# Kernel tuning notes

Hardware: AMD Instinct MI355X
Metric: run time of the kernel (lower is better)

## Reference

```python
import jax, jax.numpy as jnp
import numpy as np

N_NODES = 50000
N_EDGES = 800000
NODE_DIM = 128
EDGE_DIM = 32
HID = 64
NEG_SLOPE = 0.2  # PyG GATConv default


def _gat_layer(x, src, dst, edge_attr, W, We, a_src, a_dst, a_edge, b, n_nodes):
    """PyG GATConv with heads=1, add_self_loops=True, fill_value='mean'."""
    h = x @ W                      # [N, H] node transform (bias=False in PyG)
    he = edge_attr @ We            # [E, H] edge transform
    # self-loop edge attr = mean of incoming edge_attr per node; linearity lets
    # us take the segment-mean of the transformed he instead.
    deg = jax.ops.segment_sum(jnp.ones((src.shape[0],), h.dtype), dst, num_segments=n_nodes)
    he_loop = jax.ops.segment_sum(he, dst, num_segments=n_nodes) / jnp.maximum(deg, 1.0)[:, None]
    loop = jnp.arange(n_nodes)
    src_a = jnp.concatenate([src, loop])
    dst_a = jnp.concatenate([dst, loop])
    he_a = jnp.concatenate([he, he_loop], axis=0)
    s_src = h @ a_src              # [N]
    s_dst = h @ a_dst              # [N]
    logits = jax.nn.leaky_relu(s_src[src_a] + s_dst[dst_a] + he_a @ a_edge, NEG_SLOPE)
    # segment softmax over destination nodes (every node has a self loop)
    m = jax.ops.segment_max(logits, dst_a, num_segments=n_nodes)
    ex = jnp.exp(logits - m[dst_a])
    denom = jax.ops.segment_sum(ex, dst_a, num_segments=n_nodes)
    alpha = ex / denom[dst_a]
    out = jax.ops.segment_sum(alpha[:, None] * h[src_a], dst_a, num_segments=n_nodes)
    return out + b


def setup_inputs() -> dict:
    key = jax.random.key(0)
    ks = jax.random.split(key, 20)
    s = 0.05
    inp = {
        "x": jax.random.normal(ks[0], (N_NODES, NODE_DIM), jnp.float32),
        "edge_index": jax.random.randint(ks[1], (2, N_EDGES), 0, N_NODES, jnp.int64 if jax.config.jax_enable_x64 else jnp.int32).astype(jnp.int32),
        "edge_attr": jax.random.normal(ks[2], (N_EDGES, EDGE_DIM), jnp.float32),
        "W1": jax.random.normal(ks[3], (NODE_DIM, HID)) * s,
        "We1": jax.random.normal(ks[4], (EDGE_DIM, HID)) * s,
        "as1": jax.random.normal(ks[5], (HID,)) * s,
        "ad1": jax.random.normal(ks[6], (HID,)) * s,
        "ae1": jax.random.normal(ks[7], (HID,)) * s,
        "b1": jnp.zeros((HID,)),
        "W2": jax.random.normal(ks[8], (HID, HID)) * s,
        "We2": jax.random.normal(ks[9], (EDGE_DIM, HID)) * s,
        "as2": jax.random.normal(ks[10], (HID,)) * s,
        "ad2": jax.random.normal(ks[11], (HID,)) * s,
        "ae2": jax.random.normal(ks[12], (HID,)) * s,
        "b2": jnp.zeros((HID,)),
        "Wc1": jax.random.normal(ks[13], (2 * HID + EDGE_DIM, HID)) * s,
        "bc1": jnp.zeros((HID,)),
        "Wc2": jax.random.normal(ks[14], (HID, 1)) * s,
        "bc2": jnp.zeros((1,)),
    }
    return inp


def reference(x, edge_index, edge_attr, W1, We1, as1, ad1, ae1, b1,
              W2, We2, as2, ad2, ae2, b2, Wc1, bc1, Wc2, bc2):
    n_nodes = x.shape[0]
    row, col = edge_index[0], edge_index[1]
    x1 = jax.nn.relu(_gat_layer(x, row, col, edge_attr, W1, We1, as1, ad1, ae1, b1, n_nodes))
    x2 = jax.nn.relu(_gat_layer(x1, row, col, edge_attr, W2, We2, as2, ad2, ae2, b2, n_nodes))
    ef = jnp.concatenate([x2[row], x2[col], edge_attr], axis=-1)  # [E, 2H+De]
    h = jax.nn.relu(ef @ Wc1 + bc1)
    return (h @ Wc2 + bc2)[:, 0]
```

## Files before the change

### kernel.cpp

```cpp
#include <hip/hip_runtime.h>
#include <hip/hip_bf16.h>

#define NODE_DIM 128
#define EDGE_DIM 32
#define HID 64
#define NEG_SLOPE 0.2f

typedef __attribute__((ext_vector_type(8))) short bf16x8;
typedef __attribute__((ext_vector_type(4))) float f32x4;


template <int CTRL, int RM, int BM>
__device__ __forceinline__ float dpp_mov(float v) {
    return __int_as_float(__builtin_amdgcn_update_dpp(
        __float_as_int(v), __float_as_int(v), CTRL, RM, BM, false));
}

__device__ __forceinline__ float wave_sum63(float v) {
    v += dpp_mov<0x111, 0xf, 0xf>(v);
    v += dpp_mov<0x112, 0xf, 0xf>(v);
    v += dpp_mov<0x114, 0xf, 0xe>(v);
    v += dpp_mov<0x118, 0xf, 0xc>(v);
    v += dpp_mov<0x142, 0xa, 0xf>(v);
    v += dpp_mov<0x143, 0xc, 0xf>(v);
    return v;
}

__device__ __forceinline__ float row16_sum15(float v) {
    v += dpp_mov<0x111, 0xf, 0xf>(v);
    v += dpp_mov<0x112, 0xf, 0xf>(v);
    v += dpp_mov<0x114, 0xf, 0xe>(v);
    v += dpp_mov<0x118, 0xf, 0xc>(v);
    return v;
}

__device__ __forceinline__ float bcast63(float v) {
    return __int_as_float(__builtin_amdgcn_readlane(__float_as_int(v), 63));
}

__device__ __forceinline__ unsigned short f2bf(float f) {
    unsigned u = __float_as_uint(f);
    unsigned r = (u + 0x7fffu + ((u >> 16) & 1u)) >> 16;
    return (unsigned short)r;
}
__device__ __forceinline__ float bf2f(unsigned short h) {
    return __uint_as_float(((unsigned)h) << 16);
}


__global__ void k_count_rank_t12(const int* __restrict__ col, int* __restrict__ deg,
                                 int* __restrict__ rank, const float* __restrict__ ea,
                                 const float* __restrict__ wea1,
                                 const float* __restrict__ wea2,
                                 float2* __restrict__ t12, int E) {
    int e = blockIdx.x * 256 + threadIdx.x;
    if (e >= E) return;
    rank[e] = atomicAdd(&deg[col[e]], 1);
    const float4* e4 = (const float4*)(ea + (size_t)e * EDGE_DIM);
    const float4* w1 = (const float4*)wea1;
    const float4* w2 = (const float4*)wea2;
    float t1 = 0.f, t2 = 0.f;
#pragma unroll
    for (int k = 0; k < EDGE_DIM / 4; k++) {
        float4 v = e4[k], a = w1[k], b = w2[k];
        t1 += v.x * a.x + v.y * a.y + v.z * a.z + v.w * a.w;
        t2 += v.x * b.x + v.y * b.y + v.z * b.z + v.w * b.w;
    }
    t12[e] = make_float2(t1, t2);
}

#define SCAN_B 256
__global__ void k_scan1(const int* __restrict__ deg, int* __restrict__ tmp,
                        int* __restrict__ bsum, int N) {
    __shared__ int s[SCAN_B];
    int i = blockIdx.x * SCAN_B + threadIdx.x;
    int v = (i < N) ? deg[i] : 0;
    s[threadIdx.x] = v;
    __syncthreads();
    for (int o = 1; o < SCAN_B; o <<= 1) {
        int t = (threadIdx.x >= o) ? s[threadIdx.x - o] : 0;
        __syncthreads();
        s[threadIdx.x] += t;
        __syncthreads();
    }
    if (i < N) tmp[i] = s[threadIdx.x];
    if (threadIdx.x == SCAN_B - 1) bsum[blockIdx.x] = s[threadIdx.x];
}

__global__ void k_scan2(int* __restrict__ bsum, int nb) {
    __shared__ int s[SCAN_B];
    int v = (threadIdx.x < nb) ? bsum[threadIdx.x] : 0;
    s[threadIdx.x] = v;
    __syncthreads();
    for (int o = 1; o < SCAN_B; o <<= 1) {
        int t = (threadIdx.x >= o) ? s[threadIdx.x - o] : 0;
        __syncthreads();
        s[threadIdx.x] += t;
        __syncthreads();
    }
    if (threadIdx.x < nb) bsum[threadIdx.x] = s[threadIdx.x] - v;
}

__global__ void k_scan3(const int* __restrict__ tmp, const int* __restrict__ deg,
                        const int* __restrict__ bsum, int* __restrict__ off, int N) {
    int i = blockIdx.x * SCAN_B + threadIdx.x;
    if (i < N) off[i] = tmp[i] - deg[i] + bsum[blockIdx.x];
}

__global__ void k_wea2(const float* __restrict__ We1, const float* __restrict__ ae1,
                       const float* __restrict__ We2, const float* __restrict__ ae2,
                       float* __restrict__ wea1, float* __restrict__ wea2) {
    int t = threadIdx.x;
    const float* We = (t < 32) ? We1 : We2;
    const float* ae = (t < 32) ? ae1 : ae2;
    float* o = (t < 32) ? wea1 : wea2;
    int k = t & 31;
    float s = 0.f;
#pragma unroll
    for (int j = 0; j < HID; j++) s += We[k * HID + j] * ae[j];
    o[k] = s;
}

__global__ void k_fill_pack(const int* __restrict__ row, const int* __restrict__ col,
                            const int* __restrict__ off, const int* __restrict__ rank,
                            const float2* __restrict__ t12, const float* __restrict__ ss1,
                            float4* __restrict__ pk, int E) {
    int e = blockIdx.x * 256 + threadIdx.x;
    if (e >= E) return;
    int dn = col[e];
    int p = off[dn] + rank[e];
    float2 t = t12[e];
    int sr = row[e];
    pk[p] = make_float4(t.x, t.y, __int_as_float(sr), t.x + ss1[sr]);
}

template <int K, int NT, bool ATT, bool PQ>
__global__ __launch_bounds__(256) void k_gemm_mfma(
    const float* __restrict__ X, const float* __restrict__ W,
    const float* __restrict__ as_, const float* __restrict__ ad_,
    unsigned short* __restrict__ H, unsigned short* __restrict__ H2,
    float* __restrict__ ss, float* __restrict__ sd, int N) {
    constexpr int KC = K / 32;
    int wv = threadIdx.x >> 6, lane = threadIdx.x & 63;
    int g = lane >> 4, li = lane & 15;
    bf16x8 bhi[KC][NT], blo[KC][NT];
#pragma unroll
    for (int c = 0; c < KC; c++)
#pragma unroll
        for (int t = 0; t < NT; t++)
#pragma unroll
            for (int j = 0; j < 8; j++) {
                int k = 32 * c + 8 * g + j;
                size_t idx = (size_t)(k + ((PQ && t >= 4) ? HID : 0)) * HID + 16 * (t & 3) + li;
                float w = W[idx];
                unsigned short h = f2bf(w);
                bhi[c][t][j] = (short)h;
                blo[c][t][j] = (short)f2bf(w - bf2f(h));
            }
    float asl[NT], adl[NT];
    if (ATT) {
#pragma unroll
        for (int t = 0; t < NT; t++) {
            asl[t] = as_[16 * t + li];
            adl[t] = ad_[16 * t + li];
        }
    }
    int ntile = (N + 15) >> 4;
    for (int tb = blockIdx.x * 4 + wv; tb < ntile; tb += gridDim.x * 4) {
        int node = tb * 16 + li;
        if (node >= N) node = N - 1;
        const float* xrow = X + (size_t)node * K;
        bf16x8 ahi[KC], alo[KC];
#pragma unroll
        for (int c = 0; c < KC; c++) {
            float4 a0 = *(const float4*)(xrow + 32 * c + 8 * g);
            float4 a1 = *(const float4*)(xrow + 32 * c + 8 * g + 4);
            float xv[8] = {a0.x, a0.y, a0.z, a0.w, a1.x, a1.y, a1.z, a1.w};
#pragma unroll
            for (int j = 0; j < 8; j++) {
                unsigned short h = f2bf(xv[j]);
                ahi[c][j] = (short)h;
                alo[c][j] = (short)f2bf(xv[j] - bf2f(h));
            }
        }
        f32x4 acc[NT];
#pragma unroll
        for (int t = 0; t < NT; t++) acc[t] = (f32x4){0.f, 0.f, 0.f, 0.f};
#pragma unroll
        for (int c = 0; c < KC; c++) {
#pragma unroll
            for (int t = 0; t < NT; t++)
                acc[t] = __builtin_amdgcn_mfma_f32_16x16x32_bf16(ahi[c], bhi[c][t], acc[t], 0, 0, 0);
#pragma unroll
            for (int t = 0; t < NT; t++)
                acc[t] = __builtin_amdgcn_mfma_f32_16x16x32_bf16(ahi[c], blo[c][t], acc[t], 0, 0, 0);
#pragma unroll
            for (int t = 0; t < NT; t++)
                acc[t] = __builtin_amdgcn_mfma_f32_16x16x32_bf16(alo[c], bhi[c][t], acc[t], 0, 0, 0);
        }
        int nbase = tb * 16 + 4 * g;
#pragma unroll
        for (int t = 0; t < NT; t++) {
            unsigned short* dst = (PQ && t >= 4) ? H2 : H;
            int cofs = 16 * (t & 3) + li;
#pragma unroll
            for (int r = 0; r < 4; r++) {
                int n = nbase + r;
                if (n < N) dst[(size_t)n * HID + cofs] = f2bf(acc[t][r]);
            }
        }
        if (ATT) {
#pragma unroll
            for (int r = 0; r < 4; r++) {
                float s1 = 0.f, s2 = 0.f;
#pragma unroll
                for (int t = 0; t < NT; t++) {
                    s1 += acc[t][r] * asl[t];
                    s2 += acc[t][r] * adl[t];
                }
                s1 = row16_sum15(s1);
                s2 = row16_sum15(s2);
                int n = nbase + r;
                if (li == 15 && n < N) {
                    ss[n] = s1;
                    sd[n] = s2;
                }
            }
        }
    }
}

template <bool FOLD>
__global__ __launch_bounds__(256) void k_aggregate(
    const unsigned short* __restrict__ H, const float* __restrict__ ss,
    const float* __restrict__ sd, const float4* __restrict__ pk,
    const int* __restrict__ off, const int* __restrict__ deg,
    const float* __restrict__ b, float* __restrict__ Xo, int N) {
    __shared__ __align__(16) float2 sh[4][64];
    int wv = threadIdx.x >> 6, lane = threadIdx.x & 63;
    int n = blockIdx.x * 4 + wv;
    if (n >= N) return;
    int st = off[n], d = deg[n];
    float sdn = sd[n];
    float tsum = 0.f, dsum = 0.f, acc = 0.f;
    for (int base = 0; base < d; base += 64) {
        int i = base + lane;
        float w = 0.f;
        int s = 0;
        if (i < d) {
            float4 p = pk[st + i];
            s = __float_as_int(p.z);
            float z;
            if (FOLD) {
                tsum += p.x;
                z = p.w + sdn;
            } else {
                tsum += p.y;
                z = ss[s] + sdn + p.y;
            }
            float l = z > 0.f ? z : NEG_SLOPE * z;
            w = __expf(l);
            dsum += w;
        }
        sh[wv][lane] = make_float2(w, __int_as_float(s));
        int cnt = d - base;
        if (cnt > 64) cnt = 64;
        int j = 0;
        for (; j + 4 <= cnt; j += 4) {
            float4 a0 = *(const float4*)&sh[wv][j];
            float4 a1 = *(const float4*)&sh[wv][j + 2];
            float h0 = bf2f(H[(size_t)__float_as_int(a0.y) * HID + lane]);
            float h1 = bf2f(H[(size_t)__float_as_int(a0.w) * HID + lane]);
            float h2 = bf2f(H[(size_t)__float_as_int(a1.y) * HID + lane]);
            float h3 = bf2f(H[(size_t)__float_as_int(a1.w) * HID + lane]);
            acc += a0.x * h0 + a0.z * h1 + a1.x * h2 + a1.z * h3;
        }
        for (; j < cnt; j++) {
            float2 pr = sh[wv][j];
            acc += pr.x * bf2f(H[(size_t)__float_as_int(pr.y) * HID + lane]);
        }
    }
    tsum = bcast63(wave_sum63(tsum));
    dsum = bcast63(wave_sum63(dsum));
    float tloop = tsum / (float)(d > 1 ? d : 1);
    float zs = ss[n] + sdn + tloop;
    float lself = zs > 0.f ? zs : NEG_SLOPE * zs;
    float wself = __expf(lself);
    acc += wself * bf2f(H[(size_t)n * HID + lane]);
    dsum += wself;
    float v = acc / dsum + b[lane];
    Xo[(size_t)n * HID + lane] = fmaxf(v, 0.f);
}

__global__ __launch_bounds__(256) void k_edge_final_mfma(
    const unsigned short* __restrict__ P, const unsigned short* __restrict__ Q,
    const float* __restrict__ ea, const int* __restrict__ row,
    const int* __restrict__ col, const float* __restrict__ Wc1,
    const float* __restrict__ bc1, const float* __restrict__ Wc2,
    const float* __restrict__ bc2, float* __restrict__ out, int E) {
    int wv = threadIdx.x >> 6, lane = threadIdx.x & 63;
    int g = lane >> 4, li = lane & 15;
    bf16x8 bfrag[4];
#pragma unroll
    for (int t = 0; t < 4; t++) {
#pragma unroll
        for (int j = 0; j < 8; j++)
            bfrag[t][j] = (short)f2bf(Wc1[(size_t)(2 * HID + 8 * g + j) * HID + 16 * t + li]);
    }
    float bcv[4], wc2v[4];
#pragma unroll
    for (int t = 0; t < 4; t++) {
        bcv[t] = bc1[16 * t + li];
        wc2v[t] = Wc2[16 * t + li];
    }
    float bc2v = bc2[0];
    int ntile = (E + 15) >> 4;
    for (int tb = blockIdx.x * 4 + wv; tb < ntile; tb += gridDim.x * 4) {
        int eb = tb << 4;
        int ae_e = eb + li;
        if (ae_e >= E) ae_e = E - 1;
        const float4* ap = (const float4*)(ea + (size_t)ae_e * EDGE_DIM + 8 * g);
        float4 a0 = ap[0], a1 = ap[1];
        bf16x8 afrag;
        afrag[0] = (short)f2bf(a0.x); afrag[1] = (short)f2bf(a0.y);
        afrag[2] = (short)f2bf(a0.z); afrag[3] = (short)f2bf(a0.w);
        afrag[4] = (short)f2bf(a1.x); afrag[5] = (short)f2bf(a1.y);
        afrag[6] = (short)f2bf(a1.z); afrag[7] = (short)f2bf(a1.w);
        f32x4 acc[4];
#pragma unroll
        for (int t = 0; t < 4; t++) {
            f32x4 z = {0.f, 0.f, 0.f, 0.f};
            acc[t] = __builtin_amdgcn_mfma_f32_16x16x32_bf16(afrag, bfrag[t], z, 0, 0, 0);
        }
        int e0 = eb + 4 * g;
        int rr[4], cc[4];
        if (e0 + 3 < E) {
            int4 rv = *(const int4*)(row + e0);
            int4 cv = *(const int4*)(col + e0);
            rr[0] = rv.x; rr[1] = rv.y; rr[2] = rv.z; rr[3] = rv.w;
            cc[0] = cv.x; cc[1] = cv.y; cc[2] = cv.z; cc[3] = cv.w;
        } else {
            for (int r = 0; r < 4; r++) {
                int e = e0 + r; if (e >= E) e = E - 1;
                rr[r] = row[e]; cc[r] = col[e];
            }
        }
        float pe[4];
#pragma unroll
        for (int r = 0; r < 4; r++) {
            const unsigned short* pr = P + (size_t)rr[r] * HID;
            const unsigned short* qr = Q + (size_t)cc[r] * HID;
            float s = 0.f;
#pragma unroll
            for (int t = 0; t < 4; t++) {
                float h = acc[t][r] + bf2f(pr[16 * t + li]) + bf2f(qr[16 * t + li]) + bcv[t];
                h = fmaxf(h, 0.f);
                s += h * wc2v[t];
            }
            pe[r] = s;
        }
#pragma unroll
        for (int r = 0; r < 4; r++) pe[r] = row16_sum15(pe[r]);
        if (li == 15) {
            if (e0 + 3 < E) {
                *(float4*)(out + e0) =
                    make_float4(pe[0] + bc2v, pe[1] + bc2v, pe[2] + bc2v, pe[3] + bc2v);
            } else {
                for (int r = 0; r < 4; r++)
                    if (e0 + r < E) out[e0 + r] = pe[r] + bc2v;
            }
        }
    }
}


extern "C" void kernel_launch(void* const* d_in, const int* in_sizes, int n_in,
                              void* d_out, int out_size, void* d_ws, size_t ws_size,
                              hipStream_t stream) {
    const float* x = (const float*)d_in[0];
    const int* eidx = (const int*)d_in[1];
    const float* ea = (const float*)d_in[2];
    const float* W1 = (const float*)d_in[3];
    const float* We1 = (const float*)d_in[4];
    const float* as1 = (const float*)d_in[5];
    const float* ad1 = (const float*)d_in[6];
    const float* ae1 = (const float*)d_in[7];
    const float* b1 = (const float*)d_in[8];
    const float* W2 = (const float*)d_in[9];
    const float* We2 = (const float*)d_in[10];
    const float* as2 = (const float*)d_in[11];
    const float* ad2 = (const float*)d_in[12];
    const float* ae2 = (const float*)d_in[13];
    const float* b2 = (const float*)d_in[14];
    const float* Wc1 = (const float*)d_in[15];
    const float* bc1 = (const float*)d_in[16];
    const float* Wc2 = (const float*)d_in[17];
    const float* bc2 = (const float*)d_in[18];
    float* out = (float*)d_out;

    const int N = in_sizes[0] / NODE_DIM;
    const int E = in_sizes[1] / 2;
    const int* row = eidx;
    const int* col = eidx + E;

    char* ws = (char*)d_ws;
    size_t o = 0;
    auto carve = [&](size_t bytes) -> char* {
        char* p = ws + o;
        o += (bytes + 255) & ~(size_t)255;
        return p;
    };
    int* deg = (int*)carve((size_t)N * 4);
    int* off = (int*)carve((size_t)N * 4);
    int* tmp = (int*)carve((size_t)N * 4);
    int* bsum = (int*)carve(SCAN_B * 4);
    int* rank = (int*)carve((size_t)E * 4);
    float2* t12 = (float2*)carve((size_t)E * 8);
    float4* pk12 = (float4*)carve((size_t)E * 16);
    float* wea1 = (float*)carve(EDGE_DIM * 4);
    float* wea2 = (float*)carve(EDGE_DIM * 4);
    float* ssrc = (float*)carve((size_t)N * 4);
    float* sdst = (float*)carve((size_t)N * 4);
    unsigned short* hbuf = (unsigned short*)carve((size_t)N * HID * 2);
    unsigned short* pbuf = (unsigned short*)carve((size_t)N * HID * 2);
    float* x1 = (float*)carve((size_t)N * HID * 4);
    float* x2 = (float*)carve((size_t)N * HID * 4);
    (void)ws_size;

    const int gE = (E + 255) / 256;
    const int gN256 = (N + SCAN_B - 1) / SCAN_B;
    const int gN4 = (N + 3) / 4;
    const int gT = ((N + 15) / 16 + 3) / 4;

    (void)hipMemsetAsync(deg, 0, (size_t)N * 4, stream);
    k_wea2<<<1, 64, 0, stream>>>(We1, ae1, We2, ae2, wea1, wea2);
    k_count_rank_t12<<<gE, 256, 0, stream>>>(col, deg, rank, ea, wea1, wea2, t12, E);
    k_scan1<<<gN256, SCAN_B, 0, stream>>>(deg, tmp, bsum, N);
    k_scan2<<<1, SCAN_B, 0, stream>>>(bsum, gN256);
    k_scan3<<<gN256, SCAN_B, 0, stream>>>(tmp, deg, bsum, off, N);

    k_gemm_mfma<NODE_DIM, 4, true, false><<<gT, 256, 0, stream>>>(
        x, W1, as1, ad1, hbuf, nullptr, ssrc, sdst, N);
    k_fill_pack<<<gE, 256, 0, stream>>>(row, col, off, rank, t12, ssrc, pk12, E);

    k_aggregate<true><<<gN4, 256, 0, stream>>>(hbuf, ssrc, sdst, pk12, off, deg, b1, x1, N);

    k_gemm_mfma<HID, 4, true, false><<<gT, 256, 0, stream>>>(
        x1, W2, as2, ad2, hbuf, nullptr, ssrc, sdst, N);
    k_aggregate<false><<<gN4, 256, 0, stream>>>(hbuf, ssrc, sdst, pk12, off, deg, b2, x2, N);

    k_gemm_mfma<HID, 8, false, true><<<gT, 256, 0, stream>>>(
        x2, Wc1, nullptr, nullptr, pbuf, hbuf, nullptr, nullptr, N);
    k_edge_final_mfma<<<2048, 256, 0, stream>>>(pbuf, hbuf, ea, row, col, Wc1, bc1, Wc2, bc2, out, E);
}
```

Before: 405.9 us.

## Vectorize bf16 gathers with ushort4 loads in aggregate and edge kernels

```diff
diff --git a/kernel.cpp b/kernel.cpp
--- a/kernel.cpp
+++ b/kernel.cpp
@@ -238,11 +238,13 @@
     const float* __restrict__ b, float* __restrict__ Xo, int N) {
     __shared__ __align__(16) float2 sh[4][64];
     int wv = threadIdx.x >> 6, lane = threadIdx.x & 63;
+    int g = lane >> 4, li = lane & 15;
     int n = blockIdx.x * 4 + wv;
     if (n >= N) return;
     int st = off[n], d = deg[n];
     float sdn = sd[n];
-    float tsum = 0.f, dsum = 0.f, acc = 0.f;
+    float tsum = 0.f, dsum = 0.f;
+    float a0 = 0.f, a1 = 0.f, a2 = 0.f, a3 = 0.f;
     for (int base = 0; base < d; base += 64) {
         int i = base + lane;
         float w = 0.f;
@@ -265,19 +267,15 @@
         sh[wv][lane] = make_float2(w, __int_as_float(s));
         int cnt = d - base;
         if (cnt > 64) cnt = 64;
-        int j = 0;
-        for (; j + 4 <= cnt; j += 4) {
-            float4 a0 = *(const float4*)&sh[wv][j];
-            float4 a1 = *(const float4*)&sh[wv][j + 2];
-            float h0 = bf2f(H[(size_t)__float_as_int(a0.y) * HID + lane]);
-            float h1 = bf2f(H[(size_t)__float_as_int(a0.w) * HID + lane]);
-            float h2 = bf2f(H[(size_t)__float_as_int(a1.y) * HID + lane]);
-            float h3 = bf2f(H[(size_t)__float_as_int(a1.w) * HID + lane]);
-            acc += a0.x * h0 + a0.z * h1 + a1.x * h2 + a1.z * h3;
-        }
-        for (; j < cnt; j++) {
-            float2 pr = sh[wv][j];
-            acc += pr.x * bf2f(H[(size_t)__float_as_int(pr.y) * HID + lane]);
+        for (int j = 0; j < cnt; j += 4) {
+            int jg = j + g;
+            float2 pr = (jg < cnt) ? sh[wv][jg] : make_float2(0.f, 0.f);
+            const ushort4 hv =
+                *(const ushort4*)(H + (size_t)__float_as_int(pr.y) * HID + 4 * li);
+            a0 += pr.x * bf2f(hv.x);
+            a1 += pr.x * bf2f(hv.y);
+            a2 += pr.x * bf2f(hv.z);
+            a3 += pr.x * bf2f(hv.w);
         }
     }
     tsum = bcast63(wave_sum63(tsum));
@@ -286,10 +284,27 @@
     float zs = ss[n] + sdn + tloop;
     float lself = zs > 0.f ? zs : NEG_SLOPE * zs;
     float wself = __expf(lself);
-    acc += wself * bf2f(H[(size_t)n * HID + lane]);
     dsum += wself;
-    float v = acc / dsum + b[lane];
-    Xo[(size_t)n * HID + lane] = fmaxf(v, 0.f);
+    if (g == 0) {
+        const ushort4 hv = *(const ushort4*)(H + (size_t)n * HID + 4 * li);
+        a0 += wself * bf2f(hv.x);
+        a1 += wself * bf2f(hv.y);
+        a2 += wself * bf2f(hv.z);
+        a3 += wself * bf2f(hv.w);
+    }
+    a0 += __shfl_xor(a0, 16, 64); a0 += __shfl_xor(a0, 32, 64);
+    a1 += __shfl_xor(a1, 16, 64); a1 += __shfl_xor(a1, 32, 64);
+    a2 += __shfl_xor(a2, 16, 64); a2 += __shfl_xor(a2, 32, 64);
+    a3 += __shfl_xor(a3, 16, 64); a3 += __shfl_xor(a3, 32, 64);
+    if (g == 0) {
+        float4 bv = *(const float4*)(b + 4 * li);
+        float4 o;
+        o.x = fmaxf(a0 / dsum + bv.x, 0.f);
+        o.y = fmaxf(a1 / dsum + bv.y, 0.f);
+        o.z = fmaxf(a2 / dsum + bv.z, 0.f);
+        o.w = fmaxf(a3 / dsum + bv.w, 0.f);
+        *(float4*)(Xo + (size_t)n * HID + 4 * li) = o;
+    }
 }
 
 __global__ __launch_bounds__(256) void k_edge_final_mfma(
@@ -305,13 +320,13 @@
     for (int t = 0; t < 4; t++) {
 #pragma unroll
         for (int j = 0; j < 8; j++)
-            bfrag[t][j] = (short)f2bf(Wc1[(size_t)(2 * HID + 8 * g + j) * HID + 16 * t + li]);
+            bfrag[t][j] = (short)f2bf(Wc1[(size_t)(2 * HID + 8 * g + j) * HID + 4 * li + t]);
     }
     float bcv[4], wc2v[4];
 #pragma unroll
     for (int t = 0; t < 4; t++) {
-        bcv[t] = bc1[16 * t + li];
-        wc2v[t] = Wc2[16 * t + li];
+        bcv[t] = bc1[4 * li + t];
+        wc2v[t] = Wc2[4 * li + t];
     }
     float bc2v = bc2[0];
     int ntile = (E + 15) >> 4;
@@ -348,16 +363,14 @@
         float pe[4];
 #pragma unroll
         for (int r = 0; r < 4; r++) {
-            const unsigned short* pr = P + (size_t)rr[r] * HID;
-            const unsigned short* qr = Q + (size_t)cc[r] * HID;
-            float s = 0.f;
-#pragma unroll
-            for (int t = 0; t < 4; t++) {
-                float h = acc[t][r] + bf2f(pr[16 * t + li]) + bf2f(qr[16 * t + li]) + bcv[t];
-                h = fmaxf(h, 0.f);
-                s += h * wc2v[t];
-            }
-            pe[r] = s;
+            const ushort4 pv = *(const ushort4*)(P + (size_t)rr[r] * HID + 4 * li);
+            const ushort4 qv = *(const ushort4*)(Q + (size_t)cc[r] * HID + 4 * li);
+            float h0 = acc[0][r] + bf2f(pv.x) + bf2f(qv.x) + bcv[0];
+            float h1 = acc[1][r] + bf2f(pv.y) + bf2f(qv.y) + bcv[1];
+            float h2 = acc[2][r] + bf2f(pv.z) + bf2f(qv.z) + bcv[2];
+            float h3 = acc[3][r] + bf2f(pv.w) + bf2f(qv.w) + bcv[3];
+            pe[r] = fmaxf(h0, 0.f) * wc2v[0] + fmaxf(h1, 0.f) * wc2v[1] +
+                    fmaxf(h2, 0.f) * wc2v[2] + fmaxf(h3, 0.f) * wc2v[3];
         }
 #pragma unroll
         for (int r = 0; r < 4; r++) pe[r] = row16_sum15(pe[r]);
```

Result: no change. 413.4 us (+1.8%).

## Merge layer-1 GEMM with edge count/rank and edge-projection into one launch

Applied to the files above, without the earlier changes.

```diff
diff --git a/kernel.cpp b/kernel.cpp
--- a/kernel.cpp
+++ b/kernel.cpp
@@ -47,27 +47,6 @@
     return __uint_as_float(((unsigned)h) << 16);
 }
 
-
-__global__ void k_count_rank_t12(const int* __restrict__ col, int* __restrict__ deg,
-                                 int* __restrict__ rank, const float* __restrict__ ea,
-                                 const float* __restrict__ wea1,
-                                 const float* __restrict__ wea2,
-                                 float2* __restrict__ t12, int E) {
-    int e = blockIdx.x * 256 + threadIdx.x;
-    if (e >= E) return;
-    rank[e] = atomicAdd(&deg[col[e]], 1);
-    const float4* e4 = (const float4*)(ea + (size_t)e * EDGE_DIM);
-    const float4* w1 = (const float4*)wea1;
-    const float4* w2 = (const float4*)wea2;
-    float t1 = 0.f, t2 = 0.f;
-#pragma unroll
-    for (int k = 0; k < EDGE_DIM / 4; k++) {
-        float4 v = e4[k], a = w1[k], b = w2[k];
-        t1 += v.x * a.x + v.y * a.y + v.z * a.z + v.w * a.w;
-        t2 += v.x * b.x + v.y * b.y + v.z * b.z + v.w * b.w;
-    }
-    t12[e] = make_float2(t1, t2);
-}
 
 #define SCAN_B 256
 __global__ void k_scan1(const int* __restrict__ deg, int* __restrict__ tmp,
@@ -135,11 +114,11 @@
 }
 
 template <int K, int NT, bool ATT, bool PQ>
-__global__ __launch_bounds__(256) void k_gemm_mfma(
+__device__ __forceinline__ void gemm_body(
     const float* __restrict__ X, const float* __restrict__ W,
     const float* __restrict__ as_, const float* __restrict__ ad_,
     unsigned short* __restrict__ H, unsigned short* __restrict__ H2,
-    float* __restrict__ ss, float* __restrict__ sd, int N) {
+    float* __restrict__ ss, float* __restrict__ sd, int N, int bid, int nb) {
     constexpr int KC = K / 32;
     int wv = threadIdx.x >> 6, lane = threadIdx.x & 63;
     int g = lane >> 4, li = lane & 15;
@@ -166,7 +145,7 @@
         }
     }
     int ntile = (N + 15) >> 4;
-    for (int tb = blockIdx.x * 4 + wv; tb < ntile; tb += gridDim.x * 4) {
+    for (int tb = bid * 4 + wv; tb < ntile; tb += nb * 4) {
         int node = tb * 16 + li;
         if (node >= N) node = N - 1;
         const float* xrow = X + (size_t)node * K;
@@ -227,6 +206,54 @@
                 }
             }
         }
+    }
+}
+
+template <int K, int NT, bool ATT, bool PQ>
+__global__ __launch_bounds__(256) void k_gemm_mfma(
+    const float* __restrict__ X, const float* __restrict__ W,
+    const float* __restrict__ as_, const float* __restrict__ ad_,
+    unsigned short* __restrict__ H, unsigned short* __restrict__ H2,
+    float* __restrict__ ss, float* __restrict__ sd, int N) {
+    gemm_body<K, NT, ATT, PQ>(X, W, as_, ad_, H, H2, ss, sd, N, blockIdx.x, gridDim.x);
+}
+
+__global__ __launch_bounds__(256) void k_mega1(
+    const float* __restrict__ X, const float* __restrict__ W1,
+    const float* __restrict__ as1, const float* __restrict__ ad1,
+    unsigned short* __restrict__ H, float* __restrict__ ss, float* __restrict__ sd,
+    int N, int nbGemm,
+    const int* __restrict__ col, int* __restrict__ deg, int* __restrict__ rank,
+    int E, int nbEdge,
+    const float* __restrict__ ea, const float* __restrict__ wea1,
+    const float* __restrict__ wea2, float2* __restrict__ t12) {
+    int r = blockIdx.x;
+    int total = nbGemm + 2 * nbEdge;
+    int fr = (int)(((long long)r * nbGemm) / total);
+    int fr1 = (int)(((long long)(r + 1) * nbGemm) / total);
+    if (fr1 > fr) {
+        gemm_body<NODE_DIM, 4, true, false>(X, W1, as1, ad1, H, nullptr, ss, sd, N, fr, nbGemm);
+        return;
+    }
+    int eb = r - fr;
+    int role = eb & 1;
+    int b = eb >> 1;
+    int e = b * 256 + threadIdx.x;
+    if (e >= E) return;
+    if (role == 0) {
+        rank[e] = atomicAdd(&deg[col[e]], 1);
+    } else {
+        const float4* e4 = (const float4*)(ea + (size_t)e * EDGE_DIM);
+        const float4* w1 = (const float4*)wea1;
+        const float4* w2 = (const float4*)wea2;
+        float t1 = 0.f, t2 = 0.f;
+#pragma unroll
+        for (int k = 0; k < EDGE_DIM / 4; k++) {
+            float4 v = e4[k], a = w1[k], bb = w2[k];
+            t1 += v.x * a.x + v.y * a.y + v.z * a.z + v.w * a.w;
+            t2 += v.x * bb.x + v.y * bb.y + v.z * bb.z + v.w * bb.w;
+        }
+        t12[e] = make_float2(t1, t2);
     }
 }
 
@@ -434,13 +461,15 @@
 
     (void)hipMemsetAsync(deg, 0, (size_t)N * 4, stream);
     k_wea2<<<1, 64, 0, stream>>>(We1, ae1, We2, ae2, wea1, wea2);
-    k_count_rank_t12<<<gE, 256, 0, stream>>>(col, deg, rank, ea, wea1, wea2, t12, E);
+
+    k_mega1<<<gT + 2 * gE, 256, 0, stream>>>(
+        x, W1, as1, ad1, hbuf, ssrc, sdst, N, gT,
+        col, deg, rank, E, gE, ea, wea1, wea2, t12);
+
     k_scan1<<<gN256, SCAN_B, 0, stream>>>(deg, tmp, bsum, N);
     k_scan2<<<1, SCAN_B, 0, stream>>>(bsum, gN256);
     k_scan3<<<gN256, SCAN_B, 0, stream>>>(tmp, deg, bsum, off, N);
 
-    k_gemm_mfma<NODE_DIM, 4, true, false><<<gT, 256, 0, stream>>>(
-        x, W1, as1, ad1, hbuf, nullptr, ssrc, sdst, N);
     k_fill_pack<<<gE, 256, 0, stream>>>(row, col, off, rank, t12, ssrc, pk12, E);
 
     k_aggregate<true><<<gN4, 256, 0, stream>>>(hbuf, ssrc, sdst, pk12, off, deg, b1, x1, N);
```

New measurement: 419.4 us. 3.3% more time.

## Fuse GAT aggregation with the following node GEMM and fold the edge-weight precompute

Applied to the files above, without the earlier changes.

```diff
diff --git a/kernel.cpp b/kernel.cpp
--- a/kernel.cpp
+++ b/kernel.cpp
@@ -50,15 +50,28 @@
 
 __global__ void k_count_rank_t12(const int* __restrict__ col, int* __restrict__ deg,
                                  int* __restrict__ rank, const float* __restrict__ ea,
-                                 const float* __restrict__ wea1,
-                                 const float* __restrict__ wea2,
+                                 const float* __restrict__ We1, const float* __restrict__ ae1,
+                                 const float* __restrict__ We2, const float* __restrict__ ae2,
                                  float2* __restrict__ t12, int E) {
+    __shared__ __align__(16) float swea1[EDGE_DIM];
+    __shared__ __align__(16) float swea2[EDGE_DIM];
+    int t = threadIdx.x;
+    if (t < 64) {
+        const float* We = (t < 32) ? We1 : We2;
+        const float* ae = (t < 32) ? ae1 : ae2;
+        int k = t & 31;
+        float s = 0.f;
+#pragma unroll
+        for (int j = 0; j < HID; j++) s += We[k * HID + j] * ae[j];
+        ((t < 32) ? swea1 : swea2)[k] = s;
+    }
+    __syncthreads();
     int e = blockIdx.x * 256 + threadIdx.x;
     if (e >= E) return;
     rank[e] = atomicAdd(&deg[col[e]], 1);
     const float4* e4 = (const float4*)(ea + (size_t)e * EDGE_DIM);
-    const float4* w1 = (const float4*)wea1;
-    const float4* w2 = (const float4*)wea2;
+    const float4* w1 = (const float4*)swea1;
+    const float4* w2 = (const float4*)swea2;
     float t1 = 0.f, t2 = 0.f;
 #pragma unroll
     for (int k = 0; k < EDGE_DIM / 4; k++) {
@@ -107,20 +120,6 @@
     if (i < N) off[i] = tmp[i] - deg[i] + bsum[blockIdx.x];
 }
 
-__global__ void k_wea2(const float* __restrict__ We1, const float* __restrict__ ae1,
-                       const float* __restrict__ We2, const float* __restrict__ ae2,
-                       float* __restrict__ wea1, float* __restrict__ wea2) {
-    int t = threadIdx.x;
-    const float* We = (t < 32) ? We1 : We2;
-    const float* ae = (t < 32) ? ae1 : ae2;
-    float* o = (t < 32) ? wea1 : wea2;
-    int k = t & 31;
-    float s = 0.f;
-#pragma unroll
-    for (int j = 0; j < HID; j++) s += We[k * HID + j] * ae[j];
-    o[k] = s;
-}
-
 __global__ void k_fill_pack(const int* __restrict__ row, const int* __restrict__ col,
                             const int* __restrict__ off, const int* __restrict__ rank,
                             const float2* __restrict__ t12, const float* __restrict__ ss1,
@@ -134,12 +133,12 @@
     pk[p] = make_float4(t.x, t.y, __int_as_float(sr), t.x + ss1[sr]);
 }
 
-template <int K, int NT, bool ATT, bool PQ>
+template <int K, int NT>
 __global__ __launch_bounds__(256) void k_gemm_mfma(
     const float* __restrict__ X, const float* __restrict__ W,
     const float* __restrict__ as_, const float* __restrict__ ad_,
-    unsigned short* __restrict__ H, unsigned short* __restrict__ H2,
-    float* __restrict__ ss, float* __restrict__ sd, int N) {
+    unsigned short* __restrict__ H, float* __restrict__ ss, float* __restrict__ sd,
+    int N) {
     constexpr int KC = K / 32;
     int wv = threadIdx.x >> 6, lane = threadIdx.x & 63;
     int g = lane >> 4, li = lane & 15;
@@ -151,19 +150,17 @@
 #pragma unroll
             for (int j = 0; j < 8; j++) {
                 int k = 32 * c + 8 * g + j;
-                size_t idx = (size_t)(k + ((PQ && t >= 4) ? HID : 0)) * HID + 16 * (t & 3) + li;
+                size_t idx = (size_t)k * HID + 16 * (t & 3) + li;
                 float w = W[idx];
                 unsigned short h = f2bf(w);
                 bhi[c][t][j] = (short)h;
                 blo[c][t][j] = (short)f2bf(w - bf2f(h));
             }
     float asl[NT], adl[NT];
-    if (ATT) {
-#pragma unroll
-        for (int t = 0; t < NT; t++) {
-            asl[t] = as_[16 * t + li];
-            adl[t] = ad_[16 * t + li];
-        }
+#pragma unroll
+    for (int t = 0; t < NT; t++) {
+        asl[t] = as_[16 * t + li];
+        adl[t] = ad_[16 * t + li];
     }
     int ntile = (N + 15) >> 4;
     for (int tb = blockIdx.x * 4 + wv; tb < ntile; tb += gridDim.x * 4) {
@@ -201,95 +198,164 @@
         int nbase = tb * 16 + 4 * g;
 #pragma unroll
         for (int t = 0; t < NT; t++) {
-            unsigned short* dst = (PQ && t >= 4) ? H2 : H;
             int cofs = 16 * (t & 3) + li;
 #pragma unroll
             for (int r = 0; r < 4; r++) {
                 int n = nbase + r;
-                if (n < N) dst[(size_t)n * HID + cofs] = f2bf(acc[t][r]);
-            }
-        }
-        if (ATT) {
-#pragma unroll
-            for (int r = 0; r < 4; r++) {
-                float s1 = 0.f, s2 = 0.f;
-#pragma unroll
-                for (int t = 0; t < NT; t++) {
-                    s1 += acc[t][r] * asl[t];
-                    s2 += acc[t][r] * adl[t];
-                }
-                s1 = row16_sum15(s1);
-                s2 = row16_sum15(s2);
-                int n = nbase + r;
-                if (li == 15 && n < N) {
-                    ss[n] = s1;
-                    sd[n] = s2;
-                }
-            }
-        }
-    }
-}
-
-template <bool FOLD>
-__global__ __launch_bounds__(256) void k_aggregate(
+                if (n < N) H[(size_t)n * HID + cofs] = f2bf(acc[t][r]);
+            }
+        }
+#pragma unroll
+        for (int r = 0; r < 4; r++) {
+            float s1 = 0.f, s2 = 0.f;
+#pragma unroll
+            for (int t = 0; t < NT; t++) {
+                s1 += acc[t][r] * asl[t];
+                s2 += acc[t][r] * adl[t];
+            }
+            s1 = row16_sum15(s1);
+            s2 = row16_sum15(s2);
+            int n = nbase + r;
+            if (li == 15 && n < N) {
+                ss[n] = s1;
+                sd[n] = s2;
+            }
+        }
+    }
+}
+
+template <bool FOLD, int NT, bool ATT, bool PQ>
+__global__ __launch_bounds__(1024) void k_agg_gemm(
     const unsigned short* __restrict__ H, const float* __restrict__ ss,
     const float* __restrict__ sd, const float4* __restrict__ pk,
     const int* __restrict__ off, const int* __restrict__ deg,
-    const float* __restrict__ b, float* __restrict__ Xo, int N) {
-    __shared__ __align__(16) float2 sh[4][64];
+    const float* __restrict__ b, const float* __restrict__ W,
+    const float* __restrict__ as_, const float* __restrict__ ad_,
+    unsigned short* __restrict__ Ho, unsigned short* __restrict__ Ho2,
+    float* __restrict__ sso, float* __restrict__ sdo, int N) {
+    __shared__ __align__(16) float2 sh[16][64];
+    __shared__ __align__(16) float xt[16][68];
+    __shared__ float ps1[4][16], ps2[4][16];
     int wv = threadIdx.x >> 6, lane = threadIdx.x & 63;
-    int n = blockIdx.x * 4 + wv;
-    if (n >= N) return;
-    int st = off[n], d = deg[n];
-    float sdn = sd[n];
-    float tsum = 0.f, dsum = 0.f, acc = 0.f;
-    for (int base = 0; base < d; base += 64) {
-        int i = base + lane;
-        float w = 0.f;
-        int s = 0;
-        if (i < d) {
-            float4 p = pk[st + i];
-            s = __float_as_int(p.z);
-            float z;
-            if (FOLD) {
-                tsum += p.x;
-                z = p.w + sdn;
-            } else {
-                tsum += p.y;
-                z = ss[s] + sdn + p.y;
-            }
-            float l = z > 0.f ? z : NEG_SLOPE * z;
-            w = __expf(l);
-            dsum += w;
-        }
-        sh[wv][lane] = make_float2(w, __int_as_float(s));
-        int cnt = d - base;
-        if (cnt > 64) cnt = 64;
-        int j = 0;
-        for (; j + 4 <= cnt; j += 4) {
-            float4 a0 = *(const float4*)&sh[wv][j];
-            float4 a1 = *(const float4*)&sh[wv][j + 2];
-            float h0 = bf2f(H[(size_t)__float_as_int(a0.y) * HID + lane]);
-            float h1 = bf2f(H[(size_t)__float_as_int(a0.w) * HID + lane]);
-            float h2 = bf2f(H[(size_t)__float_as_int(a1.y) * HID + lane]);
-            float h3 = bf2f(H[(size_t)__float_as_int(a1.w) * HID + lane]);
-            acc += a0.x * h0 + a0.z * h1 + a1.x * h2 + a1.z * h3;
-        }
-        for (; j < cnt; j++) {
-            float2 pr = sh[wv][j];
-            acc += pr.x * bf2f(H[(size_t)__float_as_int(pr.y) * HID + lane]);
-        }
-    }
-    tsum = bcast63(wave_sum63(tsum));
-    dsum = bcast63(wave_sum63(dsum));
-    float tloop = tsum / (float)(d > 1 ? d : 1);
-    float zs = ss[n] + sdn + tloop;
-    float lself = zs > 0.f ? zs : NEG_SLOPE * zs;
-    float wself = __expf(lself);
-    acc += wself * bf2f(H[(size_t)n * HID + lane]);
-    dsum += wself;
-    float v = acc / dsum + b[lane];
-    Xo[(size_t)n * HID + lane] = fmaxf(v, 0.f);
+    int g = lane >> 4, li = lane & 15;
+    int nb0 = blockIdx.x * 16;
+    int n = nb0 + wv;
+    float vout = 0.f;
+    if (n < N) {
+        int st = off[n], d = deg[n];
+        float sdn = sd[n];
+        float tsum = 0.f, dsum = 0.f, acc = 0.f;
+        for (int base = 0; base < d; base += 64) {
+            int i = base + lane;
+            float w = 0.f;
+            int s = 0;
+            if (i < d) {
+                float4 p = pk[st + i];
+                s = __float_as_int(p.z);
+                float z;
+                if (FOLD) {
+                    tsum += p.x;
+                    z = p.w + sdn;
+                } else {
+                    tsum += p.y;
+                    z = ss[s] + sdn + p.y;
+                }
+                float l = z > 0.f ? z : NEG_SLOPE * z;
+                w = __expf(l);
+                dsum += w;
+            }
+            sh[wv][lane] = make_float2(w, __int_as_float(s));
+            int cnt = d - base;
+            if (cnt > 64) cnt = 64;
+            int j = 0;
+            for (; j + 4 <= cnt; j += 4) {
+                float4 a0 = *(const float4*)&sh[wv][j];
+                float4 a1 = *(const float4*)&sh[wv][j + 2];
+                float h0 = bf2f(H[(size_t)__float_as_int(a0.y) * HID + lane]);
+                float h1 = bf2f(H[(size_t)__float_as_int(a0.w) * HID + lane]);
+                float h2 = bf2f(H[(size_t)__float_as_int(a1.y) * HID + lane]);
+                float h3 = bf2f(H[(size_t)__float_as_int(a1.w) * HID + lane]);
+                acc += a0.x * h0 + a0.z * h1 + a1.x * h2 + a1.z * h3;
+            }
+            for (; j < cnt; j++) {
+                float2 pr = sh[wv][j];
+                acc += pr.x * bf2f(H[(size_t)__float_as_int(pr.y) * HID + lane]);
+            }
+        }
+        tsum = bcast63(wave_sum63(tsum));
+        dsum = bcast63(wave_sum63(dsum));
+        float tloop = tsum / (float)(d > 1 ? d : 1);
+        float zs = ss[n] + sdn + tloop;
+        float lself = zs > 0.f ? zs : NEG_SLOPE * zs;
+        float wself = __expf(lself);
+        acc += wself * bf2f(H[(size_t)n * HID + lane]);
+        dsum += wself;
+        vout = fmaxf(acc / dsum + b[lane], 0.f);
+    }
+    xt[wv][lane] = vout;
+    __syncthreads();
+    if (wv < NT) {
+        const int t = wv;
+        bf16x8 bhi[2], blo[2], ahi[2], alo[2];
+#pragma unroll
+        for (int c = 0; c < 2; c++) {
+#pragma unroll
+            for (int j = 0; j < 8; j++) {
+                int k = 32 * c + 8 * g + j;
+                size_t idx = (size_t)(k + ((PQ && t >= 4) ? HID : 0)) * HID + 16 * (t & 3) + li;
+                float w = W[idx];
+                unsigned short h = f2bf(w);
+                bhi[c][j] = (short)h;
+                blo[c][j] = (short)f2bf(w - bf2f(h));
+            }
+            float4 a0 = *(const float4*)&xt[li][32 * c + 8 * g];
+            float4 a1 = *(const float4*)&xt[li][32 * c + 8 * g + 4];
+            float xv[8] = {a0.x, a0.y, a0.z, a0.w, a1.x, a1.y, a1.z, a1.w};
+#pragma unroll
+            for (int j = 0; j < 8; j++) {
+                unsigned short h = f2bf(xv[j]);
+                ahi[c][j] = (short)h;
+                alo[c][j] = (short)f2bf(xv[j] - bf2f(h));
+            }
+        }
+        f32x4 acc = (f32x4){0.f, 0.f, 0.f, 0.f};
+#pragma unroll
+        for (int c = 0; c < 2; c++) {
+            acc = __builtin_amdgcn_mfma_f32_16x16x32_bf16(ahi[c], bhi[c], acc, 0, 0, 0);
+            acc = __builtin_amdgcn_mfma_f32_16x16x32_bf16(ahi[c], blo[c], acc, 0, 0, 0);
+            acc = __builtin_amdgcn_mfma_f32_16x16x32_bf16(alo[c], bhi[c], acc, 0, 0, 0);
+        }
+        unsigned short* dst = (PQ && t >= 4) ? Ho2 : Ho;
+        int cofs = 16 * (t & 3) + li;
+#pragma unroll
+        for (int r = 0; r < 4; r++) {
+            int nn = nb0 + 4 * g + r;
+            if (nn < N) dst[(size_t)nn * HID + cofs] = f2bf(acc[r]);
+        }
+        if (ATT) {
+            float asl = as_[16 * t + li], adl = ad_[16 * t + li];
+#pragma unroll
+            for (int r = 0; r < 4; r++) {
+                float s1 = row16_sum15(acc[r] * asl);
+                float s2 = row16_sum15(acc[r] * adl);
+                if (li == 15) {
+                    ps1[t][4 * g + r] = s1;
+                    ps2[t][4 * g + r] = s2;
+                }
+            }
+        }
+    }
+    if (ATT) {
+        __syncthreads();
+        if (threadIdx.x < 16) {
+            int nn = nb0 + threadIdx.x;
+            if (nn < N) {
+                int ti = threadIdx.x;
+                sso[nn] = ps1[0][ti] + ps1[1][ti] + ps1[2][ti] + ps1[3][ti];
+                sdo[nn] = ps2[0][ti] + ps2[1][ti] + ps2[2][ti] + ps2[3][ti];
+            }
+        }
+    }
 }
 
 __global__ __launch_bounds__(256) void k_edge_final_mfma(
@@ -417,39 +483,34 @@
     int* rank = (int*)carve((size_t)E * 4);
     float2* t12 = (float2*)carve((size_t)E * 8);
     float4* pk12 = (float4*)carve((size_t)E * 16);
-    float* wea1 = (float*)carve(EDGE_DIM * 4);
-    float* wea2 = (float*)carve(EDGE_DIM * 4);
     float* ssrc = (float*)carve((size_t)N * 4);
     float* sdst = (float*)carve((size_t)N * 4);
     unsigned short* hbuf = (unsigned short*)carve((size_t)N * HID * 2);
     unsigned short* pbuf = (unsigned short*)carve((size_t)N * HID * 2);
-    float* x1 = (float*)carve((size_t)N * HID * 4);
-    float* x2 = (float*)carve((size_t)N * HID * 4);
+    unsigned short* h2buf = (unsigned short*)carve((size_t)N * HID * 2);
     (void)ws_size;
 
     const int gE = (E + 255) / 256;
     const int gN256 = (N + SCAN_B - 1) / SCAN_B;
-    const int gN4 = (N + 3) / 4;
+    const int gB = (N + 15) / 16;
     const int gT = ((N + 15) / 16 + 3) / 4;
 
     (void)hipMemsetAsync(deg, 0, (size_t)N * 4, stream);
-    k_wea2<<<1, 64, 0, stream>>>(We1, ae1, We2, ae2, wea1, wea2);
-    k_count_rank_t12<<<gE, 256, 0, stream>>>(col, deg, rank, ea, wea1, wea2, t12, E);
+    k_count_rank_t12<<<gE, 256, 0, stream>>>(col, deg, rank, ea, We1, ae1, We2, ae2, t12, E);
     k_scan1<<<gN256, SCAN_B, 0, stream>>>(deg, tmp, bsum, N);
     k_scan2<<<1, SCAN_B, 0, stream>>>(bsum, gN256);
     k_scan3<<<gN256, SCAN_B, 0, stream>>>(tmp, deg, bsum, off, N);
 
-    k_gemm_mfma<NODE_DIM, 4, true, false><<<gT, 256, 0, stream>>>(
-        x, W1, as1, ad1, hbuf, nullptr, ssrc, sdst, N);
+    k_gemm_mfma<NODE_DIM, 4><<<gT, 256, 0, stream>>>(x, W1, as1, ad1, hbuf, ssrc, sdst, N);
     k_fill_pack<<<gE, 256, 0, stream>>>(row, col, off, rank, t12, ssrc, pk12, E);
 
-    k_aggregate<true><<<gN4, 256, 0, stream>>>(hbuf, ssrc, sdst, pk12, off, deg, b1, x1, N);
-
-    k_gemm_mfma<HID, 4, true, false><<<gT, 256, 0, stream>>>(
-        x1, W2, as2, ad2, hbuf, nullptr, ssrc, sdst, N);
-    k_aggregate<false><<<gN4, 256, 0, stream>>>(hbuf, ssrc, sdst, pk12, off, deg, b2, x2, N);
-
-    k_gemm_mfma<HID, 8, false, true><<<gT, 256, 0, stream>>>(
-        x2, Wc1, nullptr, nullptr, pbuf, hbuf, nullptr, nullptr, N);
+    k_agg_gemm<true, 4, true, false><<<gB, 1024, 0, stream>>>(
+        hbuf, ssrc, sdst, pk12, off, deg, b1, W2, as2, ad2,
+        h2buf, h2buf, ssrc, sdst, N);
+
+    k_agg_gemm<false, 8, false, true><<<gB, 1024, 0, stream>>>(
+        h2buf, ssrc, sdst, pk12, off, deg, b2, Wc1, nullptr, nullptr,
+        pbuf, hbuf, nullptr, nullptr, N);
+
     k_edge_final_mfma<<<2048, 256, 0, stream>>>(pbuf, hbuf, ea, row, col, Wc1, bc1, Wc2, bc2, out, E);
 }
```

New measurement: 450.7 us. 11.1% more time.
